# Optimization experiments

Hardware: AMD Instinct MI355X
Metric: run time of the kernel (lower is better)

## Reference

```python
import jax, jax.numpy as jnp
import numpy as np
import math

B, S, D, H = 4, 2048, 1024, 16
HD = D // H
WINDOW = 86400.0 * 7.0  # 7 days, per create_time_mask(window_size=...)


def setup_inputs() -> dict:
    key = jax.random.key(0)
    ks = jax.random.split(key, 12)
    x = jax.random.normal(ks[0], (B, S, D), dtype=jnp.float32)
    # transaction timestamps: uniform over 30 days, sorted per sequence
    timestamps = jnp.sort(jax.random.uniform(ks[1], (B, S), dtype=jnp.float32) * (86400.0 * 30.0), axis=-1)
    init = 0.02
    Wq = jax.random.normal(ks[2], (D, D), dtype=jnp.float32) * init
    bq = jnp.zeros((D,), dtype=jnp.float32)
    Wk = jax.random.normal(ks[3], (D, D), dtype=jnp.float32) * init
    bk = jnp.zeros((D,), dtype=jnp.float32)
    Wv = jax.random.normal(ks[4], (D, D), dtype=jnp.float32) * init
    bv = jnp.zeros((D,), dtype=jnp.float32)
    Wo = jax.random.normal(ks[5], (D, D), dtype=jnp.float32) * init
    bo = jnp.zeros((D,), dtype=jnp.float32)
    Wc = jax.random.normal(ks[6], (1, D), dtype=jnp.float32) * init
    bc = jnp.zeros((1,), dtype=jnp.float32)
    return {"x": x, "timestamps": timestamps, "Wq": Wq, "bq": bq, "Wk": Wk, "bk": bk,
            "Wv": Wv, "bv": bv, "Wo": Wo, "bo": bo, "Wc": Wc, "bc": bc}


def reference(x, timestamps, Wq, bq, Wk, bk, Wv, bv, Wo, bo, Wc, bc):
    b, s, d = x.shape
    scale = 1.0 / math.sqrt(HD)
    # projections (torch Linear: y = x @ W.T + b), split heads -> [b, s, H, HD]
    Q = (x @ Wq.T + bq).reshape(b, s, H, HD)
    K = (x @ Wk.T + bk).reshape(b, s, H, HD)
    V = (x @ Wv.T + bv).reshape(b, s, H, HD)
    # scores [b, H, q, k]
    scores = jnp.einsum('bqhd,bkhd->bhqk', Q, K) * scale
    # time-window mask: attend only within +/- WINDOW seconds
    time_mask = jnp.abs(timestamps[:, :, None] - timestamps[:, None, :]) <= WINDOW  # [b, s, s]
    scores = jnp.where(time_mask[:, None, :, :], scores, -jnp.inf)
    attn = jax.nn.softmax(scores, axis=-1)
    attended = jnp.einsum('bhqk,bkhd->bqhd', attn, V).reshape(b, s, d)
    output = attended @ Wo.T + bo
    change_scores = (output @ Wc.T + bc)[..., 0]  # [b, s]
    return output, change_scores
```

## Files before the change

### kernel.cpp

```cpp
#include <hip/hip_runtime.h>
#include <math.h>

#define BB 4
#define SS 2048
#define DD 1024
#define HH 16
#define HDD 64
#define NN (BB*SS)
#define WINDOWF 604800.0f
#define LOG2E 1.44269504088896340736f
#define SCALE2 (0.125f * LOG2E)
#define MSTATIC 24.0f

typedef __attribute__((ext_vector_type(8))) short bf16x8;
typedef __attribute__((ext_vector_type(4))) short bf16x4;
typedef __attribute__((ext_vector_type(4))) short s16x4;
typedef __attribute__((ext_vector_type(4))) float f32x4;

__device__ __forceinline__ unsigned short f2b(float f) {
    unsigned int x = __float_as_uint(f);
    unsigned int r = x + 0x7FFFu + ((x >> 16) & 1u);
    return (unsigned short)(r >> 16);
}

__device__ __forceinline__ unsigned int cvt_pk_bf16(float lo, float hi) {
    unsigned int r;
    asm("v_cvt_pk_bf16_f32 %0, %1, %2" : "=v"(r) : "v"(lo), "v"(hi));
    return r;
}

__device__ __forceinline__ void gload16(const unsigned short* g, unsigned short* l) {
    __builtin_amdgcn_global_load_lds(
        (const __attribute__((address_space(1))) unsigned int*)g,
        (__attribute__((address_space(3))) unsigned int*)l, 16, 0, 0);
}

__global__ __launch_bounds__(256)
void cvt_band(const float* __restrict__ x,
              const float* __restrict__ Wq, const float* __restrict__ Wk,
              const float* __restrict__ Wv, const float* __restrict__ Wo,
              const float* __restrict__ ts, const float* __restrict__ bc,
              unsigned short* __restrict__ xb,
              unsigned short* __restrict__ Wqb, unsigned short* __restrict__ Wkb,
              unsigned short* __restrict__ Wvb, unsigned short* __restrict__ Wob,
              int* __restrict__ lo, int* __restrict__ hi,
              float* __restrict__ cs)
{
    const int g = blockIdx.x;
    const int tid = threadIdx.x;
    if (g < 6144) {
        const float* src; unsigned short* dst; int i;
        if (g < 4096) { src = x; dst = xb; i = g * 2048 + tid * 8; }
        else {
            const int wi = (g - 4096) >> 9;
            src = (wi == 0) ? Wq : (wi == 1) ? Wk : (wi == 2) ? Wv : Wo;
            dst = (wi == 0) ? Wqb : (wi == 1) ? Wkb : (wi == 2) ? Wvb : Wob;
            i = ((g - 4096) & 511) * 2048 + tid * 8;
        }
        float4 v0 = *(const float4*)(src + i);
        float4 v1 = *(const float4*)(src + i + 4);
        bf16x8 o;
        o[0] = (short)f2b(v0.x); o[1] = (short)f2b(v0.y);
        o[2] = (short)f2b(v0.z); o[3] = (short)f2b(v0.w);
        o[4] = (short)f2b(v1.x); o[5] = (short)f2b(v1.y);
        o[6] = (short)f2b(v1.z); o[7] = (short)f2b(v1.w);
        *(bf16x8*)(dst + i) = o;
    } else if (g < 6176) {
        const int idx = (g - 6144) * 256 + tid;
        const int b = idx / SS, q = idx % SS;
        const float* t = ts + (size_t)b * SS;
        float tq = t[q];
        float lot = tq - WINDOWF - 1.0f;
        float hit = tq + WINDOWF + 1.0f;
        int l = 0, r = q;
        while (l < r) { int m = (l + r) >> 1; if (t[m] < lot) l = m + 1; else r = m; }
        lo[idx] = l;
        int l2 = q, r2 = SS - 1;
        while (l2 < r2) { int m = (l2 + r2 + 1) >> 1; if (t[m] > hit) r2 = m - 1; else l2 = m; }
        hi[idx] = l2;
    } else {
        const int i = (g - 6176) * 1024 + tid * 4;
        const float b0 = bc[0];
        float4 v = {b0, b0, b0, b0};
        *(float4*)(cs + i) = v;
    }
}

__device__ __forceinline__
void gemm_core(const unsigned short* __restrict__ A,
               const unsigned short* __restrict__ Bw,
               int bm, int bn, int K,
               unsigned short* As, unsigned short* Bs, f32x4 (&acc)[4][4])
{
    constexpr int BK = 64;
    const int tid = threadIdx.x;
    const int wid = tid >> 6, l = tid & 63;
    const int wm = (wid >> 1) * 64, wn = (wid & 1) * 64;
    const int lr = l & 15, lg = l >> 4;

    const int srow = l >> 3;
    const int schunk = ((l & 7) ^ srow) * 8;

    for (int k0 = 0; k0 < K; k0 += BK) {
#pragma unroll
        for (int i = 0; i < 4; ++i) {
            const int r0 = wid * 32 + i * 8;
            gload16(A  + (size_t)(bm + r0 + srow) * K + k0 + schunk, &As[r0 * BK]);
            gload16(Bw + (size_t)(bn + r0 + srow) * K + k0 + schunk, &Bs[r0 * BK]);
        }
        __syncthreads();

#pragma unroll
        for (int ks = 0; ks < 2; ++ks) {
            bf16x8 af[4], bf[4];
#pragma unroll
            for (int am = 0; am < 4; ++am) {
                const int row = wm + am * 16 + lr;
                af[am] = *(const bf16x8*)&As[row * BK + (((ks * 4 + lg) ^ (row & 7)) * 8)];
            }
#pragma unroll
            for (int nf = 0; nf < 4; ++nf) {
                const int row = wn + nf * 16 + lr;
                bf[nf] = *(const bf16x8*)&Bs[row * BK + (((ks * 4 + lg) ^ (row & 7)) * 8)];
            }
#pragma unroll
            for (int am = 0; am < 4; ++am)
#pragma unroll
                for (int nf = 0; nf < 4; ++nf)
                    acc[am][nf] = __builtin_amdgcn_mfma_f32_16x16x32_bf16(
                        af[am], bf[nf], acc[am][nf], 0, 0, 0);
        }
        __syncthreads();
    }
}

__global__ __launch_bounds__(256)
void gemm_qk(const unsigned short* __restrict__ xb,
             const unsigned short* __restrict__ Wqb,
             const unsigned short* __restrict__ Wkb,
             const float* __restrict__ bq, const float* __restrict__ bk,
             unsigned short* __restrict__ Qb, unsigned short* __restrict__ Kb2)
{
    __shared__ unsigned short As[128 * 64];
    __shared__ unsigned short Bs[128 * 64];

    const int seg = blockIdx.y >> 3;
    const int bm = blockIdx.x * 128;
    const int bn = (blockIdx.y & 7) * 128;
    const unsigned short* Bw = seg ? Wkb : Wqb;
    const float* bias = seg ? bk : bq;
    unsigned short* Y = seg ? Kb2 : Qb;
    const float alpha = seg ? 1.0f : SCALE2;

    f32x4 acc[4][4];
#pragma unroll
    for (int i = 0; i < 4; ++i)
#pragma unroll
        for (int j = 0; j < 4; ++j) acc[i][j] = (f32x4){0.f, 0.f, 0.f, 0.f};

    gemm_core(xb, Bw, bm, bn, DD, As, Bs, acc);

    const int l = threadIdx.x & 63, wid = threadIdx.x >> 6;
    const int wm = (wid >> 1) * 64, wn = (wid & 1) * 64;
    const int lr = l & 15, lg = l >> 4;
    float bia[4];
#pragma unroll
    for (int nf = 0; nf < 4; ++nf) bia[nf] = bias[bn + wn + nf * 16 + lr];

#pragma unroll
    for (int am = 0; am < 4; ++am)
#pragma unroll
        for (int nf = 0; nf < 4; ++nf)
#pragma unroll
            for (int r = 0; r < 4; ++r) {
                float o = (acc[am][nf][r] + bia[nf]) * alpha;
                size_t m = (size_t)(bm + wm + am * 16 + lg * 4 + r);
                size_t n = (size_t)(bn + wn + nf * 16 + lr);
                Y[m * DD + n] = f2b(o);
            }
}

__global__ __launch_bounds__(256)
void gemm_v(const unsigned short* __restrict__ xb,
            const unsigned short* __restrict__ Wvb,
            const float* __restrict__ bv, unsigned short* __restrict__ Vtb)
{
    __shared__ unsigned short As[128 * 64];
    __shared__ unsigned short Bs[128 * 64];

    const int bm = blockIdx.x * 128;
    const int bn = blockIdx.y * 128;

    f32x4 acc[4][4];
#pragma unroll
    for (int i = 0; i < 4; ++i)
#pragma unroll
        for (int j = 0; j < 4; ++j) acc[i][j] = (f32x4){0.f, 0.f, 0.f, 0.f};

    gemm_core(xb, Wvb, bm, bn, DD, As, Bs, acc);

    const int l = threadIdx.x & 63, wid = threadIdx.x >> 6;
    const int wm = (wid >> 1) * 64, wn = (wid & 1) * 64;
    const int lr = l & 15, lg = l >> 4;
    float bia[4];
#pragma unroll
    for (int nf = 0; nf < 4; ++nf) bia[nf] = bv[bn + wn + nf * 16 + lr];

#pragma unroll
    for (int am = 0; am < 4; ++am)
#pragma unroll
        for (int nf = 0; nf < 4; ++nf) {
            int mbase = bm + wm + am * 16 + lg * 4;
            int n = bn + wn + nf * 16 + lr;
            int bidx = mbase >> 11, sidx = mbase & (SS - 1);
            s16x4 o;
#pragma unroll
            for (int r = 0; r < 4; ++r)
                o[r] = (short)f2b(acc[am][nf][r] + bia[nf]);
            *(s16x4*)(Vtb + (((size_t)(bidx << 10) + n) << 11) + sidx) = o;
        }
}

__global__ __launch_bounds__(256)
void gemm_wo_change(const unsigned short* __restrict__ A,
                    const unsigned short* __restrict__ Bw,
                    const float* __restrict__ bias,
                    float* __restrict__ Y,
                    const float* __restrict__ Wc,
                    float* __restrict__ cs)
{
    __shared__ unsigned short As[128 * 64];
    __shared__ unsigned short Bs[128 * 64];

    const int bm = blockIdx.x * 128;
    const int bn = blockIdx.y * 128;

    f32x4 acc[4][4];
#pragma unroll
    for (int i = 0; i < 4; ++i)
#pragma unroll
        for (int j = 0; j < 4; ++j) acc[i][j] = (f32x4){0.f, 0.f, 0.f, 0.f};

    gemm_core(A, Bw, bm, bn, DD, As, Bs, acc);

    const int l = threadIdx.x & 63, wid = threadIdx.x >> 6;
    const int wm = (wid >> 1) * 64, wn = (wid & 1) * 64;
    const int lr = l & 15, lg = l >> 4;

    float bia[4], wcv[4];
#pragma unroll
    for (int nf = 0; nf < 4; ++nf) {
        bia[nf] = bias[bn + wn + nf * 16 + lr];
        wcv[nf] = Wc[bn + wn + nf * 16 + lr];
    }

    float csum[4][4];
#pragma unroll
    for (int am = 0; am < 4; ++am)
#pragma unroll
        for (int r = 0; r < 4; ++r) csum[am][r] = 0.f;

#pragma unroll
    for (int am = 0; am < 4; ++am)
#pragma unroll
        for (int nf = 0; nf < 4; ++nf)
#pragma unroll
            for (int r = 0; r < 4; ++r) {
                float o = acc[am][nf][r] + bia[nf];
                size_t m = (size_t)(bm + wm + am * 16 + lg * 4 + r);
                size_t n = (size_t)(bn + wn + nf * 16 + lr);
                Y[m * DD + n] = o;
                csum[am][r] = fmaf(o, wcv[nf], csum[am][r]);
            }

#pragma unroll
    for (int am = 0; am < 4; ++am)
#pragma unroll
        for (int r = 0; r < 4; ++r) {
            float v = csum[am][r];
            v += __shfl_xor(v, 1);
            v += __shfl_xor(v, 2);
            v += __shfl_xor(v, 4);
            v += __shfl_xor(v, 8);
            if (lr == 0)
                atomicAdd(&cs[bm + wm + am * 16 + lg * 4 + r], v);
        }
}

__global__ __launch_bounds__(256)
void attn_mfma(const unsigned short* __restrict__ Qb, const unsigned short* __restrict__ Kb,
               const unsigned short* __restrict__ Vt, const float* __restrict__ Tg,
               const int* __restrict__ lo, const int* __restrict__ hi,
               unsigned short* __restrict__ Ab)
{
    __shared__ unsigned short Ks[2][64 * 64];
    __shared__ unsigned short Vs[2][64 * 64];

    const int blk = blockIdx.x;
    const int xcd = blk & 7;
    const int idx = blk >> 3;
    const int bh  = xcd * 8 + (idx >> 5);
    const int i5  = idx & 31;
    const int qt  = (i5 & 1) ? (15 - (i5 >> 1)) : (16 + (i5 >> 1));
    const int b = bh >> 4, h = bh & 15;

    const int tid = threadIdx.x;
    const int wid = tid >> 6, l = tid & 63;
    const int lr = l & 15, lg = l >> 4;
    const int q0w = qt * 64 + wid * 16;

    const size_t qrow = (size_t)(b * SS + q0w + lr);
    const bf16x8 qf0 = *(const bf16x8*)(Qb + qrow * DD + h * HDD + lg * 8);
    const bf16x8 qf1 = *(const bf16x8*)(Qb + qrow * DD + h * HDD + 32 + lg * 8);

    const float* tb = Tg + (size_t)b * SS;
    const float tq = tb[q0w + lr];
    const float tq_min = tb[qt * 64];
    const float tq_max = tb[qt * 64 + 63];

    const int t0 = lo[b * SS + qt * 64] >> 6;
    const int t1 = hi[b * SS + qt * 64 + 63] >> 6;

    const unsigned short* Kbh = Kb + (size_t)b * SS * DD + h * HDD;
    const unsigned short* Vth = Vt + ((size_t)(b * 1024 + h * HDD)) * SS;

    const int srow = l >> 3;
    const int schunk = (((l & 7) - srow) & 7) * 8;

    const unsigned short* kg0 = Kbh + (size_t)(t0 * 64 + wid * 16 + srow) * DD + schunk;
    const unsigned short* kg1 = kg0 + 8 * DD;
    const unsigned short* vg0 = Vth + (size_t)(wid * 16 + srow) * SS + t0 * 64 + schunk;
    const unsigned short* vg1 = vg0 + 8 * SS;

    const int ka_off = lr * 64 + (((lg + lr) & 7) << 3);
    const int c0 = lg >> 1, h4 = (lg & 1) * 4;
    const int pv0 = lr * 64 + (((c0 + 0 + lr) & 7) << 3) + h4;
    const int pv1 = lr * 64 + (((c0 + 2 + lr) & 7) << 3) + h4;
    const int pv2 = lr * 64 + (((c0 + 4 + lr) & 7) << 3) + h4;
    const int pv3 = lr * 64 + (((c0 + 6 + lr) & 7) << 3) + h4;

    bf16x8 onesv;
#pragma unroll
    for (int j = 0; j < 8; ++j) onesv[j] = (short)0x3F80;

    unsigned short *Kc = &Ks[0][0], *Kn = &Ks[1][0];
    unsigned short *Vc = &Vs[0][0], *Vn = &Vs[1][0];

    float l_ = 0.f;
    f32x4 o_[4];
#pragma unroll
    for (int df = 0; df < 4; ++df) o_[df] = (f32x4){0.f, 0.f, 0.f, 0.f};

    gload16(kg0, Kc + wid * 1024);
    gload16(kg1, Kc + wid * 1024 + 512);
    gload16(vg0, Vc + wid * 1024);
    gload16(vg1, Vc + wid * 1024 + 512);
    kg0 += 64 * DD; kg1 += 64 * DD; vg0 += 64; vg1 += 64;
    __syncthreads();

    for (int t = t0; t <= t1; ++t) {
        const int kk0 = t * 64;

        if (t < t1) {
            gload16(kg0, Kn + wid * 1024);
            gload16(kg1, Kn + wid * 1024 + 512);
            gload16(vg0, Vn + wid * 1024);
            gload16(vg1, Vn + wid * 1024 + 512);
            kg0 += 64 * DD; kg1 += 64 * DD; vg0 += 64; vg1 += 64;
        }

        f32x4 s[4];
        __builtin_amdgcn_s_setprio(1);
#pragma unroll
        for (int kf = 0; kf < 4; ++kf) {
            bf16x8 ka0 = *(const bf16x8*)(Kc + kf * 1024 + ka_off);
            bf16x8 ka1 = *(const bf16x8*)(Kc + kf * 1024 + (ka_off ^ 32));
            f32x4 z = (f32x4){-MSTATIC, -MSTATIC, -MSTATIC, -MSTATIC};
            z = __builtin_amdgcn_mfma_f32_16x16x32_bf16(ka0, qf0, z, 0, 0, 0);
            z = __builtin_amdgcn_mfma_f32_16x16x32_bf16(ka1, qf1, z, 0, 0, 0);
            s[kf] = z;
        }
        __builtin_amdgcn_s_setprio(0);

        const bool needmask = !((tq_max - tb[kk0] <= WINDOWF - 4.0f) &&
                                (tb[kk0 + 63] - tq_min <= WINDOWF - 4.0f));
        if (needmask) {
#pragma unroll
            for (int kf = 0; kf < 4; ++kf) {
                float4 tk4 = *(const float4*)(tb + kk0 + kf * 16 + lg * 4);
                if (!(fabsf(tq - tk4.x) <= WINDOWF)) s[kf][0] = -INFINITY;
                if (!(fabsf(tq - tk4.y) <= WINDOWF)) s[kf][1] = -INFINITY;
                if (!(fabsf(tq - tk4.z) <= WINDOWF)) s[kf][2] = -INFINITY;
                if (!(fabsf(tq - tk4.w) <= WINDOWF)) s[kf][3] = -INFINITY;
            }
        }

#pragma unroll
        for (int kf = 0; kf < 4; ++kf)
#pragma unroll
            for (int r = 0; r < 4; ++r)
                s[kf][r] = __builtin_amdgcn_exp2f(s[kf][r]);

        union { unsigned int u[4]; bf16x8 v; } pb[2];
#pragma unroll
        for (int c = 0; c < 2; ++c) {
            pb[c].u[0] = cvt_pk_bf16(s[2 * c][0],     s[2 * c][1]);
            pb[c].u[1] = cvt_pk_bf16(s[2 * c][2],     s[2 * c][3]);
            pb[c].u[2] = cvt_pk_bf16(s[2 * c + 1][0], s[2 * c + 1][1]);
            pb[c].u[3] = cvt_pk_bf16(s[2 * c + 1][2], s[2 * c + 1][3]);
        }

        __builtin_amdgcn_s_setprio(1);
        {
            f32x4 zl = (f32x4){0.f, 0.f, 0.f, 0.f};
            zl = __builtin_amdgcn_mfma_f32_16x16x32_bf16(onesv, pb[0].v, zl, 0, 0, 0);
            zl = __builtin_amdgcn_mfma_f32_16x16x32_bf16(onesv, pb[1].v, zl, 0, 0, 0);
            l_ += zl[0];
        }

#pragma unroll
        for (int df = 0; df < 4; ++df) {
            const int base = df * 1024;
            union { bf16x4 hh[2]; bf16x8 v; } va0, va1;
            va0.hh[0] = *(const bf16x4*)(Vc + base + pv0);
            va0.hh[1] = *(const bf16x4*)(Vc + base + pv1);
            va1.hh[0] = *(const bf16x4*)(Vc + base + pv2);
            va1.hh[1] = *(const bf16x4*)(Vc + base + pv3);
            o_[df] = __builtin_amdgcn_mfma_f32_16x16x32_bf16(va0.v, pb[0].v, o_[df], 0, 0, 0);
            o_[df] = __builtin_amdgcn_mfma_f32_16x16x32_bf16(va1.v, pb[1].v, o_[df], 0, 0, 0);
        }
        __builtin_amdgcn_s_setprio(0);

        __syncthreads();
        unsigned short* tk = Kc; Kc = Kn; Kn = tk;
        unsigned short* tv = Vc; Vc = Vn; Vn = tv;
    }

    const float inv = 1.f / l_;
#pragma unroll
    for (int df = 0; df < 4; ++df) {
        s16x4 o;
#pragma unroll
        for (int r = 0; r < 4; ++r) o[r] = (short)f2b(o_[df][r] * inv);
        *(s16x4*)(Ab + qrow * DD + h * HDD + df * 16 + lg * 4) = o;
    }
}

extern "C" void kernel_launch(void* const* d_in, const int* in_sizes, int n_in,
                              void* d_out, int out_size, void* d_ws, size_t ws_size,
                              hipStream_t stream)
{
    (void)in_sizes; (void)n_in; (void)out_size; (void)ws_size;
    const float* x  = (const float*)d_in[0];
    const float* ts = (const float*)d_in[1];
    const float* Wq = (const float*)d_in[2];
    const float* bq = (const float*)d_in[3];
    const float* Wk = (const float*)d_in[4];
    const float* bk = (const float*)d_in[5];
    const float* Wv = (const float*)d_in[6];
    const float* bv = (const float*)d_in[7];
    const float* Wo = (const float*)d_in[8];
    const float* bo = (const float*)d_in[9];
    const float* Wc = (const float*)d_in[10];
    const float* bc = (const float*)d_in[11];

    float* out = (float*)d_out;
    float* cs  = out + (size_t)NN * DD;

    unsigned short* xb  = (unsigned short*)d_ws;
    unsigned short* Qb  = xb  + (size_t)NN * DD;
    unsigned short* Kb2 = Qb  + (size_t)NN * DD;
    unsigned short* Vtb = Kb2 + (size_t)NN * DD;
    unsigned short* Abf = Vtb + (size_t)NN * DD;
    unsigned short* Wqb = Abf + (size_t)NN * DD;
    unsigned short* Wkb = Wqb + (size_t)DD * DD;
    unsigned short* Wvb = Wkb + (size_t)DD * DD;
    unsigned short* Wob = Wvb + (size_t)DD * DD;
    int* lo = (int*)(Wob + (size_t)DD * DD);
    int* hi = lo + NN;

    cvt_band<<<6184, 256, 0, stream>>>(x, Wq, Wk, Wv, Wo, ts, bc,
                                       xb, Wqb, Wkb, Wvb, Wob, lo, hi, cs);

    gemm_qk<<<dim3(NN / 128, 16), 256, 0, stream>>>(xb, Wqb, Wkb, bq, bk, Qb, Kb2);
    gemm_v<<<dim3(NN / 128, DD / 128), 256, 0, stream>>>(xb, Wvb, bv, Vtb);

    attn_mfma<<<BB * HH * (SS / 64), 256, 0, stream>>>(Qb, Kb2, Vtb, ts, lo, hi, Abf);
    gemm_wo_change<<<dim3(NN / 128, DD / 128), 256, 0, stream>>>(Abf, Wob, bo, out, Wc, cs);
}
```

Baseline: 171.5 us.

## Split attention waves into 2 query-tiles by 2 key-halves with LDS reduction

Each wave now processes two 16-row query tiles against half of the 64-key block instead of one query tile against the full block. Each K and V fragment read from LDS therefore feeds two MFMAs, which halves LDS read traffic per MFMA. The partial outputs and row sums from the two key halves are combined through shared memory at the end. This costs more registers for the doubled accumulators, two extra barriers, and a store/load reduction step.

```diff
diff --git a/kernel.cpp b/kernel.cpp
--- a/kernel.cpp
+++ b/kernel.cpp
@@ -307,14 +307,20 @@
     const int tid = threadIdx.x;
     const int wid = tid >> 6, l = tid & 63;
     const int lr = l & 15, lg = l >> 4;
-    const int q0w = qt * 64 + wid * 16;
-
-    const size_t qrow = (size_t)(b * SS + q0w + lr);
-    const bf16x8 qf0 = *(const bf16x8*)(Qb + qrow * DD + h * HDD + lg * 8);
-    const bf16x8 qf1 = *(const bf16x8*)(Qb + qrow * DD + h * HDD + 32 + lg * 8);
+    const int qs = wid >> 1;
+    const int kh = wid & 1;
+    const int q0w = qt * 64 + qs * 32;
+
+    const size_t rowA = (size_t)(b * SS + q0w + lr);
+    const size_t rowB = (size_t)(b * SS + q0w + 16 + lr);
+    const bf16x8 qfA0 = *(const bf16x8*)(Qb + rowA * DD + h * HDD + lg * 8);
+    const bf16x8 qfA1 = *(const bf16x8*)(Qb + rowA * DD + h * HDD + 32 + lg * 8);
+    const bf16x8 qfB0 = *(const bf16x8*)(Qb + rowB * DD + h * HDD + lg * 8);
+    const bf16x8 qfB1 = *(const bf16x8*)(Qb + rowB * DD + h * HDD + 32 + lg * 8);
 
     const float* tb = Tg + (size_t)b * SS;
-    const float tq = tb[q0w + lr];
+    const float tqA = tb[q0w + lr];
+    const float tqB = tb[q0w + 16 + lr];
     const float tq_min = tb[qt * 64];
     const float tq_max = tb[qt * 64 + 63];
 
@@ -332,12 +338,11 @@
     const unsigned short* vg0 = Vth + (size_t)(wid * 16 + srow) * SS + t0 * 64 + schunk;
     const unsigned short* vg1 = vg0 + 8 * SS;
 
+    const int kbase = kh * 2048;
     const int ka_off = lr * 64 + (((lg + lr) & 7) << 3);
     const int c0 = lg >> 1, h4 = (lg & 1) * 4;
-    const int pv0 = lr * 64 + (((c0 + 0 + lr) & 7) << 3) + h4;
-    const int pv1 = lr * 64 + (((c0 + 2 + lr) & 7) << 3) + h4;
-    const int pv2 = lr * 64 + (((c0 + 4 + lr) & 7) << 3) + h4;
-    const int pv3 = lr * 64 + (((c0 + 6 + lr) & 7) << 3) + h4;
+    const int pv0 = lr * 64 + (((c0 + kh * 4 + 0 + lr) & 7) << 3) + h4;
+    const int pv1 = lr * 64 + (((c0 + kh * 4 + 2 + lr) & 7) << 3) + h4;
 
     bf16x8 onesv;
 #pragma unroll
@@ -346,10 +351,13 @@
     unsigned short *Kc = &Ks[0][0], *Kn = &Ks[1][0];
     unsigned short *Vc = &Vs[0][0], *Vn = &Vs[1][0];
 
-    float l_ = 0.f;
-    f32x4 o_[4];
-#pragma unroll
-    for (int df = 0; df < 4; ++df) o_[df] = (f32x4){0.f, 0.f, 0.f, 0.f};
+    float lA = 0.f, lB = 0.f;
+    f32x4 oA[4], oB[4];
+#pragma unroll
+    for (int df = 0; df < 4; ++df) {
+        oA[df] = (f32x4){0.f, 0.f, 0.f, 0.f};
+        oB[df] = (f32x4){0.f, 0.f, 0.f, 0.f};
+    }
 
     gload16(kg0, Kc + wid * 1024);
     gload16(kg1, Kc + wid * 1024 + 512);
@@ -369,16 +377,20 @@
             kg0 += 64 * DD; kg1 += 64 * DD; vg0 += 64; vg1 += 64;
         }
 
-        f32x4 s[4];
+        f32x4 sA[2], sB[2];
         __builtin_amdgcn_s_setprio(1);
 #pragma unroll
-        for (int kf = 0; kf < 4; ++kf) {
-            bf16x8 ka0 = *(const bf16x8*)(Kc + kf * 1024 + ka_off);
-            bf16x8 ka1 = *(const bf16x8*)(Kc + kf * 1024 + (ka_off ^ 32));
-            f32x4 z = (f32x4){-MSTATIC, -MSTATIC, -MSTATIC, -MSTATIC};
-            z = __builtin_amdgcn_mfma_f32_16x16x32_bf16(ka0, qf0, z, 0, 0, 0);
-            z = __builtin_amdgcn_mfma_f32_16x16x32_bf16(ka1, qf1, z, 0, 0, 0);
-            s[kf] = z;
+        for (int kf = 0; kf < 2; ++kf) {
+            bf16x8 ka0 = *(const bf16x8*)(Kc + kbase + kf * 1024 + ka_off);
+            bf16x8 ka1 = *(const bf16x8*)(Kc + kbase + kf * 1024 + (ka_off ^ 32));
+            f32x4 zA = (f32x4){-MSTATIC, -MSTATIC, -MSTATIC, -MSTATIC};
+            zA = __builtin_amdgcn_mfma_f32_16x16x32_bf16(ka0, qfA0, zA, 0, 0, 0);
+            zA = __builtin_amdgcn_mfma_f32_16x16x32_bf16(ka1, qfA1, zA, 0, 0, 0);
+            sA[kf] = zA;
+            f32x4 zB = (f32x4){-MSTATIC, -MSTATIC, -MSTATIC, -MSTATIC};
+            zB = __builtin_amdgcn_mfma_f32_16x16x32_bf16(ka0, qfB0, zB, 0, 0, 0);
+            zB = __builtin_amdgcn_mfma_f32_16x16x32_bf16(ka1, qfB1, zB, 0, 0, 0);
+            sB[kf] = zB;
         }
         __builtin_amdgcn_s_setprio(0);
 
@@ -386,48 +398,55 @@
                                 (tb[kk0 + 63] - tq_min <= WINDOWF - 4.0f));
         if (needmask) {
 #pragma unroll
-            for (int kf = 0; kf < 4; ++kf) {
-                float4 tk4 = *(const float4*)(tb + kk0 + kf * 16 + lg * 4);
-                if (!(fabsf(tq - tk4.x) <= WINDOWF)) s[kf][0] = -INFINITY;
-                if (!(fabsf(tq - tk4.y) <= WINDOWF)) s[kf][1] = -INFINITY;
-                if (!(fabsf(tq - tk4.z) <= WINDOWF)) s[kf][2] = -INFINITY;
-                if (!(fabsf(tq - tk4.w) <= WINDOWF)) s[kf][3] = -INFINITY;
-            }
-        }
-
-#pragma unroll
-        for (int kf = 0; kf < 4; ++kf)
-#pragma unroll
-            for (int r = 0; r < 4; ++r)
-                s[kf][r] = __builtin_amdgcn_exp2f(s[kf][r]);
-
-        union { unsigned int u[4]; bf16x8 v; } pb[2];
-#pragma unroll
-        for (int c = 0; c < 2; ++c) {
-            pb[c].u[0] = cvt_pk_bf16(s[2 * c][0],     s[2 * c][1]);
-            pb[c].u[1] = cvt_pk_bf16(s[2 * c][2],     s[2 * c][3]);
-            pb[c].u[2] = cvt_pk_bf16(s[2 * c + 1][0], s[2 * c + 1][1]);
-            pb[c].u[3] = cvt_pk_bf16(s[2 * c + 1][2], s[2 * c + 1][3]);
-        }
+            for (int kf = 0; kf < 2; ++kf) {
+                float4 tk4 = *(const float4*)(tb + kk0 + kh * 32 + kf * 16 + lg * 4);
+                if (!(fabsf(tqA - tk4.x) <= WINDOWF)) sA[kf][0] = -INFINITY;
+                if (!(fabsf(tqA - tk4.y) <= WINDOWF)) sA[kf][1] = -INFINITY;
+                if (!(fabsf(tqA - tk4.z) <= WINDOWF)) sA[kf][2] = -INFINITY;
+                if (!(fabsf(tqA - tk4.w) <= WINDOWF)) sA[kf][3] = -INFINITY;
+                if (!(fabsf(tqB - tk4.x) <= WINDOWF)) sB[kf][0] = -INFINITY;
+                if (!(fabsf(tqB - tk4.y) <= WINDOWF)) sB[kf][1] = -INFINITY;
+                if (!(fabsf(tqB - tk4.z) <= WINDOWF)) sB[kf][2] = -INFINITY;
+                if (!(fabsf(tqB - tk4.w) <= WINDOWF)) sB[kf][3] = -INFINITY;
+            }
+        }
+
+#pragma unroll
+        for (int kf = 0; kf < 2; ++kf)
+#pragma unroll
+            for (int r = 0; r < 4; ++r) {
+                sA[kf][r] = __builtin_amdgcn_exp2f(sA[kf][r]);
+                sB[kf][r] = __builtin_amdgcn_exp2f(sB[kf][r]);
+            }
+
+        union { unsigned int u[4]; bf16x8 v; } pbA, pbB;
+        pbA.u[0] = cvt_pk_bf16(sA[0][0], sA[0][1]);
+        pbA.u[1] = cvt_pk_bf16(sA[0][2], sA[0][3]);
+        pbA.u[2] = cvt_pk_bf16(sA[1][0], sA[1][1]);
+        pbA.u[3] = cvt_pk_bf16(sA[1][2], sA[1][3]);
+        pbB.u[0] = cvt_pk_bf16(sB[0][0], sB[0][1]);
+        pbB.u[1] = cvt_pk_bf16(sB[0][2], sB[0][3]);
+        pbB.u[2] = cvt_pk_bf16(sB[1][0], sB[1][1]);
+        pbB.u[3] = cvt_pk_bf16(sB[1][2], sB[1][3]);
 
         __builtin_amdgcn_s_setprio(1);
         {
             f32x4 zl = (f32x4){0.f, 0.f, 0.f, 0.f};
-            zl = __builtin_amdgcn_mfma_f32_16x16x32_bf16(onesv, pb[0].v, zl, 0, 0, 0);
-            zl = __builtin_amdgcn_mfma_f32_16x16x32_bf16(onesv, pb[1].v, zl, 0, 0, 0);
-            l_ += zl[0];
+            zl = __builtin_amdgcn_mfma_f32_16x16x32_bf16(onesv, pbA.v, zl, 0, 0, 0);
+            lA += zl[0];
+            f32x4 zb = (f32x4){0.f, 0.f, 0.f, 0.f};
+            zb = __builtin_amdgcn_mfma_f32_16x16x32_bf16(onesv, pbB.v, zb, 0, 0, 0);
+            lB += zb[0];
         }
 
 #pragma unroll
         for (int df = 0; df < 4; ++df) {
             const int base = df * 1024;
-            union { bf16x4 hh[2]; bf16x8 v; } va0, va1;
-            va0.hh[0] = *(const bf16x4*)(Vc + base + pv0);
-            va0.hh[1] = *(const bf16x4*)(Vc + base + pv1);
-            va1.hh[0] = *(const bf16x4*)(Vc + base + pv2);
-            va1.hh[1] = *(const bf16x4*)(Vc + base + pv3);
-            o_[df] = __builtin_amdgcn_mfma_f32_16x16x32_bf16(va0.v, pb[0].v, o_[df], 0, 0, 0);
-            o_[df] = __builtin_amdgcn_mfma_f32_16x16x32_bf16(va1.v, pb[1].v, o_[df], 0, 0, 0);
+            union { bf16x4 hh[2]; bf16x8 v; } va;
+            va.hh[0] = *(const bf16x4*)(Vc + base + pv0);
+            va.hh[1] = *(const bf16x4*)(Vc + base + pv1);
+            oA[df] = __builtin_amdgcn_mfma_f32_16x16x32_bf16(va.v, pbA.v, oA[df], 0, 0, 0);
+            oB[df] = __builtin_amdgcn_mfma_f32_16x16x32_bf16(va.v, pbB.v, oB[df], 0, 0, 0);
         }
         __builtin_amdgcn_s_setprio(0);
 
@@ -436,13 +455,42 @@
         unsigned short* tv = Vc; Vc = Vn; Vn = tv;
     }
 
-    const float inv = 1.f / l_;
-#pragma unroll
-    for (int df = 0; df < 4; ++df) {
-        s16x4 o;
-#pragma unroll
-        for (int r = 0; r < 4; ++r) o[r] = (short)f2b(o_[df][r] * inv);
-        *(s16x4*)(Ab + qrow * DD + h * HDD + df * 16 + lg * 4) = o;
+    float* red  = (float*)&Ks[0][0];
+    float* lbuf = red + 64 * 64;
+    __syncthreads();
+    if (kh == 1) {
+#pragma unroll
+        for (int df = 0; df < 4; ++df) {
+            *(f32x4*)&red[(qs * 32 + lr) * 64 + df * 16 + lg * 4]      = oA[df];
+            *(f32x4*)&red[(qs * 32 + 16 + lr) * 64 + df * 16 + lg * 4] = oB[df];
+        }
+        if (lg == 0) {
+            lbuf[qs * 32 + lr]      = lA;
+            lbuf[qs * 32 + 16 + lr] = lB;
+        }
+    }
+    __syncthreads();
+    if (kh == 0) {
+#pragma unroll
+        for (int df = 0; df < 4; ++df) {
+            f32x4 a = *(const f32x4*)&red[(qs * 32 + lr) * 64 + df * 16 + lg * 4];
+            f32x4 bv_ = *(const f32x4*)&red[(qs * 32 + 16 + lr) * 64 + df * 16 + lg * 4];
+#pragma unroll
+            for (int r = 0; r < 4; ++r) { oA[df][r] += a[r]; oB[df][r] += bv_[r]; }
+        }
+        const float invA = 1.f / (lA + lbuf[qs * 32 + lr]);
+        const float invB = 1.f / (lB + lbuf[qs * 32 + 16 + lr]);
+#pragma unroll
+        for (int df = 0; df < 4; ++df) {
+            s16x4 a, bo_;
+#pragma unroll
+            for (int r = 0; r < 4; ++r) {
+                a[r]   = (short)f2b(oA[df][r] * invA);
+                bo_[r] = (short)f2b(oB[df][r] * invB);
+            }
+            *(s16x4*)(Ab + rowA * DD + h * HDD + df * 16 + lg * 4) = a;
+            *(s16x4*)(Ab + rowB * DD + h * HDD + df * 16 + lg * 4) = bo_;
+        }
     }
 }
 
```

Result: slower. 177.6 us (+3.5%).
